# Kernel tuning notes

Measured on AMD Instinct MI355X. Metric: run time of the kernel, lower is better.

## Reference

```python
import jax, jax.numpy as jnp
import numpy as np

N = 50000       # nodes
E = 800000      # edges (before self-loops)
IN_DIM = 256
HID = 64
HEADS = 3
N_CLASSES = 40
NEG_SLOPE = 0.2  # PyG GATConv default negative_slope


def setup_inputs() -> dict:
    key = jax.random.key(0)
    ks = jax.random.split(key, 12)
    x = jax.random.normal(ks[0], (N, IN_DIM), jnp.float32)
    src = jax.random.randint(ks[1], (E,), 0, N, dtype=jnp.int32)
    off = jax.random.randint(ks[2], (E,), 1, N, dtype=jnp.int32)
    dst = (src + off) % N  # guarantees no self-loops
    edge_index = jnp.stack([src, dst], axis=0)
    g = 0.1
    W1 = jax.random.normal(ks[3], (IN_DIM, HEADS * HID), jnp.float32) * g
    att_src1 = jax.random.normal(ks[4], (HEADS, HID), jnp.float32) * g
    att_dst1 = jax.random.normal(ks[5], (HEADS, HID), jnp.float32) * g
    b1 = jnp.zeros((HEADS * HID,), jnp.float32)
    W2 = jax.random.normal(ks[6], (HEADS * HID, HEADS * HID), jnp.float32) * g
    att_src2 = jax.random.normal(ks[7], (HEADS, HID), jnp.float32) * g
    att_dst2 = jax.random.normal(ks[8], (HEADS, HID), jnp.float32) * g
    b2 = jnp.zeros((HEADS * HID,), jnp.float32)
    Wout = jax.random.normal(ks[9], (HEADS * HID, N_CLASSES), jnp.float32) * g
    bout = jnp.zeros((N_CLASSES,), jnp.float32)
    return {"x": x, "edge_index": edge_index,
            "W1": W1, "att_src1": att_src1, "att_dst1": att_dst1, "b1": b1,
            "W2": W2, "att_src2": att_src2, "att_dst2": att_dst2, "b2": b2,
            "Wout": Wout, "bout": bout}


def _segment_softmax(logits, seg, num_segments):
    # logits: [E', H], seg: [E'] destination node ids
    m = jax.ops.segment_max(logits, seg, num_segments=num_segments)
    e = jnp.exp(logits - m[seg])
    s = jax.ops.segment_sum(e, seg, num_segments=num_segments)
    return e / s[seg]


def _gat_layer(x, src, dst, W, att_src, att_dst, bias):
    n = x.shape[0]
    h = (x @ W).reshape(n, HEADS, HID)               # lin_src == lin_dst (x is a Tensor)
    a_src = jnp.sum(h * att_src, axis=-1)            # [N, H]
    a_dst = jnp.sum(h * att_dst, axis=-1)            # [N, H]
    alpha = jax.nn.leaky_relu(a_src[src] + a_dst[dst], NEG_SLOPE)  # [E', H]
    alpha = _segment_softmax(alpha, dst, n)
    msg = h[src] * alpha[:, :, None]                 # [E', H, C]
    out = jax.ops.segment_sum(msg, dst, num_segments=n)  # scatter-add aggregate
    return out.reshape(n, HEADS * HID) + bias        # concat heads + bias


def reference(x, edge_index, W1, att_src1, att_dst1, b1,
              W2, att_src2, att_dst2, b2, Wout, bout):
    n = x.shape[0]
    loop = jnp.arange(n, dtype=edge_index.dtype)
    src = jnp.concatenate([edge_index[0], loop])     # add_self_loops=True
    dst = jnp.concatenate([edge_index[1], loop])
    h = _gat_layer(x, src, dst, W1, att_src1, att_dst1, b1)
    h = jax.nn.relu(h)                               # dropout p=0 -> identity
    h = _gat_layer(h, src, dst, W2, att_src2, att_dst2, b2)
    h = jax.nn.relu(h)
    return h @ Wout + bout                           # node-level readout + outlayer
```

## Files before the change

### kernel.cpp

```cpp
#include <hip/hip_runtime.h>
#include <math.h>

#define NN 50000
#define NE 800000
#define KIN 256
#define F 192
#define NH 3
#define NC 40
#define CNT_BLKS ((NE+255)/256)
#define CONV_N (F*KIN + F*F + 48*F)
#define CONV_BLKS ((CONV_N+255)/256)
#define GEMM_GRID_C ((NN+63)/64)
#define EMIT_BLKS 49

typedef unsigned short u16;
typedef unsigned int   u32;
typedef __attribute__((ext_vector_type(8))) short bf16x8;
typedef __attribute__((ext_vector_type(4))) float f32x4;

static __device__ __forceinline__ u16 f2bf(float f){
  u32 u = __float_as_uint(f);
  u32 r = (u + 0x7fffu + ((u >> 16) & 1u)) >> 16;
  return (u16)r;
}

__global__ void count_conv_kernel(const int* __restrict__ dst, int* __restrict__ cnt,
                                  const float* __restrict__ W1, const float* __restrict__ W2,
                                  const float* __restrict__ Wout,
                                  u16* __restrict__ w1t, u16* __restrict__ w2t, u16* __restrict__ wot){
  int b = blockIdx.x;
  if (b < CNT_BLKS){
    int e = b*256 + threadIdx.x;
    if (e < NE) atomicAdd(&cnt[dst[e]], 1);
    return;
  }
  int e = (b - CNT_BLKS)*256 + threadIdx.x;
  if (e < F*KIN){
    int c = e / KIN, r = e % KIN;
    w1t[e] = f2bf(W1[(size_t)r*F + c]);
    return;
  }
  int e2 = e - F*KIN;
  if (e2 < F*F){
    int c = e2 / F, r = e2 % F;
    w2t[e2] = f2bf(W2[(size_t)r*F + c]);
    return;
  }
  int e3 = e2 - F*F;
  if (e3 < 48*F){
    int n = e3 / F, k = e3 % F;
    wot[e3] = (n < NC)? f2bf(Wout[(size_t)k*NC + n]) : (u16)0;
  }
}

__global__ __launch_bounds__(256) void emit_all(int* __restrict__ cnt, int* __restrict__ row_ptr){
  __shared__ int ts[256];
  __shared__ int s_pred;
  const int b = blockIdx.x, t = threadIdx.x;
  const int lim = b*1024;
  int pred = 0;
  for (int i = t*4; i < lim; i += 1024){
    int4 v = *(const int4*)&cnt[i];
    pred += v.x + v.y + v.z + v.w;
  }
  ts[t] = pred;
  __syncthreads();
  for (int off=128; off; off>>=1){
    if (t < off) ts[t] += ts[t+off];
    __syncthreads();
  }
  if (t == 0) s_pred = ts[0];
  __syncthreads();
  const int base = lim + t*4;
  int4 v = make_int4(0,0,0,0);
  if (base + 3 < NN) v = *(const int4*)&cnt[base];
  else if (base < NN){
    v.x = cnt[base];
    if (base+1 < NN) v.y = cnt[base+1];
    if (base+2 < NN) v.z = cnt[base+2];
  }
  int tot = v.x + v.y + v.z + v.w;
  ts[t] = tot;
  __syncthreads();
  #pragma unroll
  for (int off=1; off<256; off<<=1){
    int val = (t >= off)? ts[t-off] : 0;
    __syncthreads();
    ts[t] += val;
    __syncthreads();
  }
  int off0 = s_pred + ts[t] - tot;
  if (base + 3 < NN){
    row_ptr[base]   = off0;
    row_ptr[base+1] = off0 + v.x;
    row_ptr[base+2] = off0 + v.x + v.y;
    row_ptr[base+3] = off0 + v.x + v.y + v.z;
    *(int4*)&cnt[base] = make_int4(0,0,0,0);
  } else if (base < NN){
    row_ptr[base] = off0; cnt[base] = 0;
    if (base+1 < NN){ row_ptr[base+1] = off0 + v.x; cnt[base+1] = 0; }
    if (base+2 < NN){ row_ptr[base+2] = off0 + v.x + v.y; cnt[base+2] = 0; }
  }
  if (b == 0 && t == 0) row_ptr[NN] = NE;
}

#define SAK 72
#define SC  196
template<int K, bool CONVA, bool FILL>
__global__ __launch_bounds__(256) void gemm_mfma(const void* __restrict__ Araw, const u16* __restrict__ Bt,
                                                 u16* __restrict__ C,
                                                 const float* __restrict__ att_src, const float* __restrict__ att_dst,
                                                 float* __restrict__ a_src4, float* __restrict__ a_dst4,
                                                 const int* __restrict__ fsrc, const int* __restrict__ fdst,
                                                 const int* __restrict__ row_ptr, int* __restrict__ cur,
                                                 int* __restrict__ col){
  if (FILL && blockIdx.x >= GEMM_GRID_C){
    int e = (blockIdx.x - GEMM_GRID_C)*256 + threadIdx.x;
    if (e < NE){
      int d = fdst[e];
      int p = row_ptr[d] + atomicAdd(&cur[d], 1);
      col[p] = fsrc[e];
    }
    return;
  }
  __shared__ __align__(16) union {
    struct { u16 As[64*SAK]; u16 Bs[192*SAK]; } st;
    u16 Cs[64*SC];
  } sh;
  const int t = threadIdx.x;
  const int wave = t >> 6, lane = t & 63;
  const int quad = lane >> 4, l16 = lane & 15;
  const int r0 = blockIdx.x*64;

  f32x4 acc[4][3];
  #pragma unroll
  for (int rt=0;rt<4;rt++)
    #pragma unroll
    for (int ct=0;ct<3;ct++) acc[rt][ct] = (f32x4){0.f,0.f,0.f,0.f};

  for (int k0=0; k0<K; k0+=64){
    __syncthreads();
    {
      int row = t >> 2, kq = (t & 3)*16;
      bool ok = (r0+row) < NN;
      if (CONVA){
        const float* Af = (const float*)Araw;
        float4 v0 = make_float4(0,0,0,0), v1 = v0, v2 = v0, v3 = v0;
        if (ok){
          const float* p = &Af[(size_t)(r0+row)*K + k0 + kq];
          v0 = *(const float4*)(p+0);
          v1 = *(const float4*)(p+4);
          v2 = *(const float4*)(p+8);
          v3 = *(const float4*)(p+12);
        }
        uint4 pa, pb;
        pa.x = (u32)f2bf(v0.x) | ((u32)f2bf(v0.y) << 16);
        pa.y = (u32)f2bf(v0.z) | ((u32)f2bf(v0.w) << 16);
        pa.z = (u32)f2bf(v1.x) | ((u32)f2bf(v1.y) << 16);
        pa.w = (u32)f2bf(v1.z) | ((u32)f2bf(v1.w) << 16);
        pb.x = (u32)f2bf(v2.x) | ((u32)f2bf(v2.y) << 16);
        pb.y = (u32)f2bf(v2.z) | ((u32)f2bf(v2.w) << 16);
        pb.z = (u32)f2bf(v3.x) | ((u32)f2bf(v3.y) << 16);
        pb.w = (u32)f2bf(v3.z) | ((u32)f2bf(v3.w) << 16);
        *(uint4*)&sh.st.As[row*SAK + kq]     = pa;
        *(uint4*)&sh.st.As[row*SAK + kq + 8] = pb;
      } else {
        const u16* Ab = (const u16*)Araw;
        uint4 va = make_uint4(0,0,0,0), vb = va;
        if (ok){
          va = *(const uint4*)&Ab[(size_t)(r0+row)*K + k0 + kq];
          vb = *(const uint4*)&Ab[(size_t)(r0+row)*K + k0 + kq + 8];
        }
        *(uint4*)&sh.st.As[row*SAK + kq]     = va;
        *(uint4*)&sh.st.As[row*SAK + kq + 8] = vb;
      }
    }
    #pragma unroll
    for (int i=0;i<6;i++){
      int idx = t + i*256;
      int n = idx >> 3, kc = idx & 7;
      *(uint4*)&sh.st.Bs[n*SAK + kc*8] = *(const uint4*)&Bt[(size_t)n*K + k0 + kc*8];
    }
    __syncthreads();
    bf16x8 af[4][2], bf[3][2];
    #pragma unroll
    for (int kf=0;kf<2;kf++){
      #pragma unroll
      for (int rt=0;rt<4;rt++) af[rt][kf] = *(const bf16x8*)&sh.st.As[(rt*16 + l16)*SAK + kf*32 + quad*8];
      #pragma unroll
      for (int ct=0;ct<3;ct++) bf[ct][kf] = *(const bf16x8*)&sh.st.Bs[(wave*48 + ct*16 + l16)*SAK + kf*32 + quad*8];
    }
    #pragma unroll
    for (int kf=0;kf<2;kf++)
      #pragma unroll
      for (int rt=0;rt<4;rt++)
        #pragma unroll
        for (int ct=0;ct<3;ct++)
          acc[rt][ct] = __builtin_amdgcn_mfma_f32_16x16x32_bf16(af[rt][kf], bf[ct][kf], acc[rt][ct], 0, 0, 0);
  }

  __syncthreads();
  #pragma unroll
  for (int ct=0;ct<3;ct++){
    const int n = wave*48 + ct*16 + l16;
    #pragma unroll
    for (int rt=0;rt<4;rt++){
      #pragma unroll
      for (int reg=0;reg<4;reg++){
        const int m = rt*16 + quad*4 + reg;
        sh.Cs[m*SC + n] = f2bf(acc[rt][ct][reg]);
      }
    }
  }
  __syncthreads();
  {
    int row = t >> 2, c0 = (t & 3)*6;
    int grow = r0 + row;
    if (grow < NN){
      #pragma unroll
      for (int j=0;j<6;j++){
        int ch = c0 + j;
        uint4 v = *(const uint4*)&sh.Cs[row*SC + ch*8];
        *(uint4*)&C[(size_t)grow*F + ch*8] = v;
      }
    }
  }
  if (t < 192){
    int row = t & 63, head = t >> 6;
    int grow = r0 + row;
    if (grow < NN){
      float ps = 0.f, pd = 0.f;
      #pragma unroll
      for (int j=0;j<8;j++){
        uint4 v = *(const uint4*)&sh.Cs[row*SC + head*64 + j*8];
        float4 w0 = *(const float4*)&att_src[head*64 + j*8];
        float4 w1 = *(const float4*)&att_src[head*64 + j*8 + 4];
        float4 d0 = *(const float4*)&att_dst[head*64 + j*8];
        float4 d1 = *(const float4*)&att_dst[head*64 + j*8 + 4];
        float c0f = __uint_as_float(v.x << 16), c1f = __uint_as_float(v.x & 0xffff0000u);
        float c2f = __uint_as_float(v.y << 16), c3f = __uint_as_float(v.y & 0xffff0000u);
        float c4f = __uint_as_float(v.z << 16), c5f = __uint_as_float(v.z & 0xffff0000u);
        float c6f = __uint_as_float(v.w << 16), c7f = __uint_as_float(v.w & 0xffff0000u);
        ps = fmaf(c0f,w0.x,fmaf(c1f,w0.y,fmaf(c2f,w0.z,fmaf(c3f,w0.w,ps))));
        ps = fmaf(c4f,w1.x,fmaf(c5f,w1.y,fmaf(c6f,w1.z,fmaf(c7f,w1.w,ps))));
        pd = fmaf(c0f,d0.x,fmaf(c1f,d0.y,fmaf(c2f,d0.z,fmaf(c3f,d0.w,pd))));
        pd = fmaf(c4f,d1.x,fmaf(c5f,d1.y,fmaf(c6f,d1.z,fmaf(c7f,d1.w,pd))));
      }
      a_src4[(size_t)grow*4 + head] = ps;
      a_dst4[(size_t)grow*4 + head] = pd;
    }
  }
}

__global__ __launch_bounds__(256) void gat_agg_wave(const u16* __restrict__ hb,
    const float* __restrict__ a_src4, const float* __restrict__ a_dst4,
    const int* __restrict__ row_ptr, const int* __restrict__ col,
    const float* __restrict__ bias, u16* __restrict__ out){
  __shared__ float s_al[4][64][4];
  const int t = threadIdx.x;
  const int lane = t & 63;
  const int w = t >> 6;
  const int d = blockIdx.x*4 + w;
  if (d >= NN) return;
  const int e0  = row_ptr[d];
  const int deg = row_ptr[d+1] - e0;
  const int ecount = deg + 1;
  const float4 ad = *(const float4*)&a_dst4[(size_t)d*4];

  const int cg = (lane < 48)? lane : lane - 48;
  const int hg = (lane < 48)? (lane >> 4) : 0;
  const int cgo = cg*4;
  float4 acc = make_float4(0.f,0.f,0.f,0.f);
  float sl0=0.f, sl1=0.f, sl2=0.f;

  for (int base=0; base<ecount; base+=64){
    int j = base + lane;
    bool valid = j < ecount;
    int sn = d;
    if (j < deg) sn = col[e0+j];
    float4 as = *(const float4*)&a_src4[(size_t)sn*4];
    float l0 = as.x + ad.x; l0 = (l0>0.f)? l0 : 0.2f*l0;
    float l1 = as.y + ad.y; l1 = (l1>0.f)? l1 : 0.2f*l1;
    float l2 = as.z + ad.z; l2 = (l2>0.f)? l2 : 0.2f*l2;
    float E0 = valid? __expf(l0) : 0.f;
    float E1 = valid? __expf(l1) : 0.f;
    float E2 = valid? __expf(l2) : 0.f;
    sl0 += E0; sl1 += E1; sl2 += E2;
    float4 st; st.x = E0; st.y = E1; st.z = E2; st.w = 0.f;
    *(float4*)&s_al[w][lane][0] = st;
    __builtin_amdgcn_wave_barrier();
    int cnt = ecount - base; if (cnt > 64) cnt = 64;
    int jj = 0;
    for (; jj+4 <= cnt; jj += 4){
      int sA = __builtin_amdgcn_readlane(sn, jj);
      int sB = __builtin_amdgcn_readlane(sn, jj+1);
      int sC = __builtin_amdgcn_readlane(sn, jj+2);
      int sD = __builtin_amdgcn_readlane(sn, jj+3);
      uint2 pA = *(const uint2*)(hb + sA*F + cgo);
      uint2 pB = *(const uint2*)(hb + sB*F + cgo);
      uint2 pC = *(const uint2*)(hb + sC*F + cgo);
      uint2 pD = *(const uint2*)(hb + sD*F + cgo);
      float aA = s_al[w][jj  ][hg];
      float aB = s_al[w][jj+1][hg];
      float aC = s_al[w][jj+2][hg];
      float aD = s_al[w][jj+3][hg];
      acc.x = fmaf(aA, __uint_as_float(pA.x << 16),         acc.x);
      acc.y = fmaf(aA, __uint_as_float(pA.x & 0xffff0000u), acc.y);
      acc.z = fmaf(aA, __uint_as_float(pA.y << 16),         acc.z);
      acc.w = fmaf(aA, __uint_as_float(pA.y & 0xffff0000u), acc.w);
      acc.x = fmaf(aB, __uint_as_float(pB.x << 16),         acc.x);
      acc.y = fmaf(aB, __uint_as_float(pB.x & 0xffff0000u), acc.y);
      acc.z = fmaf(aB, __uint_as_float(pB.y << 16),         acc.z);
      acc.w = fmaf(aB, __uint_as_float(pB.y & 0xffff0000u), acc.w);
      acc.x = fmaf(aC, __uint_as_float(pC.x << 16),         acc.x);
      acc.y = fmaf(aC, __uint_as_float(pC.x & 0xffff0000u), acc.y);
      acc.z = fmaf(aC, __uint_as_float(pC.y << 16),         acc.z);
      acc.w = fmaf(aC, __uint_as_float(pC.y & 0xffff0000u), acc.w);
      acc.x = fmaf(aD, __uint_as_float(pD.x << 16),         acc.x);
      acc.y = fmaf(aD, __uint_as_float(pD.x & 0xffff0000u), acc.y);
      acc.z = fmaf(aD, __uint_as_float(pD.y << 16),         acc.z);
      acc.w = fmaf(aD, __uint_as_float(pD.y & 0xffff0000u), acc.w);
    }
    for (; jj < cnt; jj++){
      int sA = __builtin_amdgcn_readlane(sn, jj);
      uint2 pA = *(const uint2*)(hb + sA*F + cgo);
      float aA = s_al[w][jj][hg];
      acc.x = fmaf(aA, __uint_as_float(pA.x << 16),         acc.x);
      acc.y = fmaf(aA, __uint_as_float(pA.x & 0xffff0000u), acc.y);
      acc.z = fmaf(aA, __uint_as_float(pA.y << 16),         acc.z);
      acc.w = fmaf(aA, __uint_as_float(pA.y & 0xffff0000u), acc.w);
    }
    __builtin_amdgcn_wave_barrier();
  }
  #pragma unroll
  for (int off=32; off; off>>=1){
    sl0 += __shfl_xor(sl0, off);
    sl1 += __shfl_xor(sl1, off);
    sl2 += __shfl_xor(sl2, off);
  }
  if (lane < 48){
    float inv = 1.f / ((hg==0)? sl0 : ((hg==1)? sl1 : sl2));
    float4 b4 = *(const float4*)&bias[cg*4];
    uint2 o;
    o.x = (u32)f2bf(fmaxf(fmaf(acc.x, inv, b4.x), 0.f))
        | ((u32)f2bf(fmaxf(fmaf(acc.y, inv, b4.y), 0.f)) << 16);
    o.y = (u32)f2bf(fmaxf(fmaf(acc.z, inv, b4.z), 0.f))
        | ((u32)f2bf(fmaxf(fmaf(acc.w, inv, b4.w), 0.f)) << 16);
    *(uint2*)&out[(size_t)d*F + cg*4] = o;
  }
}

__global__ __launch_bounds__(256) void gemm_out_mfma(const u16* __restrict__ A,
    const u16* __restrict__ Wt, const float* __restrict__ bias, float* __restrict__ out){
  const int t = threadIdx.x;
  const int wave = t >> 6, lane = t & 63;
  const int quad = lane >> 4, l16 = lane & 15;
  const int rbase = blockIdx.x*64 + wave*16;
  const int arow = rbase + l16;
  f32x4 acc[3];
  #pragma unroll
  for (int ct=0;ct<3;ct++) acc[ct] = (f32x4){0.f,0.f,0.f,0.f};
  #pragma unroll
  for (int ks=0; ks<6; ks++){
    const int k0 = ks*32;
    union { uint4 u; bf16x8 h; } cva;
    cva.u = make_uint4(0,0,0,0);
    if (arow < NN) cva.u = *(const uint4*)&A[(size_t)arow*F + k0 + quad*8];
    #pragma unroll
    for (int ct=0;ct<3;ct++){
      bf16x8 bfr = *(const bf16x8*)&Wt[(size_t)(ct*16 + l16)*F + k0 + quad*8];
      acc[ct] = __builtin_amdgcn_mfma_f32_16x16x32_bf16(cva.h, bfr, acc[ct], 0, 0, 0);
    }
  }
  #pragma unroll
  for (int ct=0;ct<3;ct++){
    const int n = ct*16 + l16;
    #pragma unroll
    for (int reg=0;reg<4;reg++){
      const int m = quad*4 + reg;
      const int grow = rbase + m;
      if (grow < NN && n < NC) out[(size_t)grow*NC + n] = acc[ct][reg] + bias[n];
    }
  }
}

extern "C" void kernel_launch(void* const* d_in, const int* in_sizes, int n_in,
                              void* d_out, int out_size, void* d_ws, size_t ws_size,
                              hipStream_t stream){
  const float* x    = (const float*)d_in[0];
  const int*   ei   = (const int*)  d_in[1];
  const float* W1   = (const float*)d_in[2];
  const float* as1  = (const float*)d_in[3];
  const float* ad1  = (const float*)d_in[4];
  const float* b1   = (const float*)d_in[5];
  const float* W2   = (const float*)d_in[6];
  const float* as2  = (const float*)d_in[7];
  const float* ad2  = (const float*)d_in[8];
  const float* b2   = (const float*)d_in[9];
  const float* Wout = (const float*)d_in[10];
  const float* bout = (const float*)d_in[11];
  float* out = (float*)d_out;

  u16* w1t = (u16*)d_ws;
  u16* w2t = w1t + (size_t)F*KIN;
  u16* wot = w2t + (size_t)F*F;
  u16* hb1 = wot + (size_t)48*F;
  u16* hb2 = hb1 + (size_t)NN*F;
  u16* gb1 = hb2 + (size_t)NN*F;
  u16* gb2 = gb1 + (size_t)NN*F;
  float* a_src4 = (float*)(gb2 + (size_t)NN*F);
  float* a_dst4 = a_src4 + (size_t)NN*4;
  int* row_ptr  = (int*)(a_dst4 + (size_t)NN*4);
  int* col      = row_ptr + (NN+1);
  int* cnt      = col + NE;

  const int* srcv = ei;
  const int* dstv = ei + NE;

  hipMemsetAsync(cnt, 0, NN*sizeof(int), stream);
  count_conv_kernel<<<CNT_BLKS + CONV_BLKS, 256, 0, stream>>>(dstv, cnt, W1, W2, Wout, w1t, w2t, wot);
  emit_all<<<EMIT_BLKS, 256, 0, stream>>>(cnt, row_ptr);

  const int AGG_GRID = (NN + 3)/4;
  gemm_mfma<KIN,true,true><<<GEMM_GRID_C + CNT_BLKS, 256, 0, stream>>>(
      x, w1t, hb1, as1, ad1, a_src4, a_dst4, srcv, dstv, row_ptr, cnt, col);
  gat_agg_wave<<<AGG_GRID, 256, 0, stream>>>(hb1, a_src4, a_dst4, row_ptr, col, b1, gb1);
  gemm_mfma<F,false,false><<<GEMM_GRID_C, 256, 0, stream>>>(
      gb1, w2t, hb2, as2, ad2, a_src4, a_dst4, nullptr, nullptr, nullptr, nullptr, nullptr);
  gat_agg_wave<<<AGG_GRID, 256, 0, stream>>>(hb2, a_src4, a_dst4, row_ptr, col, b2, gb2);
  gemm_out_mfma<<<GEMM_GRID_C, 256, 0, stream>>>(gb2, wot, bout, out);
}
```

Measured before the change: 338.5 us.

## Pre-pack weights into MFMA fragment layout and load B directly from global

The weight conversion kernel now writes W1 and W2 in a k-blocked packed layout (groups of 8 k values per output column), so each lane can fetch its bf16x8 B fragment with one global load. The GEMM kernel stops staging B tiles in shared memory, which shrinks LDS use and removes the B store/load traffic. B fragments are issued before the A staging so their latency can overlap it. The cost is that each wave reads B from global/L2 independently instead of sharing it through LDS.

```diff
diff --git a/kernel.cpp b/kernel.cpp
--- a/kernel.cpp
+++ b/kernel.cpp
@@ -8,7 +8,7 @@
 #define NH 3
 #define NC 40
 #define CNT_BLKS ((NE+255)/256)
-#define CONV_N (F*KIN + F*F + 48*F)
+#define CONV_N (KIN*F + F*F + 48*F)
 #define CONV_BLKS ((CONV_N+255)/256)
 #define GEMM_GRID_C ((NN+63)/64)
 #define EMIT_BLKS 49
@@ -27,7 +27,7 @@
 __global__ void count_conv_kernel(const int* __restrict__ dst, int* __restrict__ cnt,
                                   const float* __restrict__ W1, const float* __restrict__ W2,
                                   const float* __restrict__ Wout,
-                                  u16* __restrict__ w1t, u16* __restrict__ w2t, u16* __restrict__ wot){
+                                  u16* __restrict__ w1p, u16* __restrict__ w2p, u16* __restrict__ wot){
   int b = blockIdx.x;
   if (b < CNT_BLKS){
     int e = b*256 + threadIdx.x;
@@ -35,15 +35,15 @@
     return;
   }
   int e = (b - CNT_BLKS)*256 + threadIdx.x;
-  if (e < F*KIN){
-    int c = e / KIN, r = e % KIN;
-    w1t[e] = f2bf(W1[(size_t)r*F + c]);
+  if (e < KIN*F){
+    int k = e / F, n = e % F;
+    w1p[((size_t)(k>>3)*F + n)*8 + (k&7)] = f2bf(W1[e]);
     return;
   }
-  int e2 = e - F*KIN;
+  int e2 = e - KIN*F;
   if (e2 < F*F){
-    int c = e2 / F, r = e2 % F;
-    w2t[e2] = f2bf(W2[(size_t)r*F + c]);
+    int k = e2 / F, n = e2 % F;
+    w2p[((size_t)(k>>3)*F + n)*8 + (k&7)] = f2bf(W2[e2]);
     return;
   }
   int e3 = e2 - F*F;
@@ -107,7 +107,7 @@
 #define SAK 72
 #define SC  196
 template<int K, bool CONVA, bool FILL>
-__global__ __launch_bounds__(256) void gemm_mfma(const void* __restrict__ Araw, const u16* __restrict__ Bt,
+__global__ __launch_bounds__(256) void gemm_mfma(const void* __restrict__ Araw, const u16* __restrict__ Bp,
                                                  u16* __restrict__ C,
                                                  const float* __restrict__ att_src, const float* __restrict__ att_dst,
                                                  float* __restrict__ a_src4, float* __restrict__ a_dst4,
@@ -124,7 +124,7 @@
     return;
   }
   __shared__ __align__(16) union {
-    struct { u16 As[64*SAK]; u16 Bs[192*SAK]; } st;
+    u16 As[64*SAK];
     u16 Cs[64*SC];
   } sh;
   const int t = threadIdx.x;
@@ -138,8 +138,18 @@
     #pragma unroll
     for (int ct=0;ct<3;ct++) acc[rt][ct] = (f32x4){0.f,0.f,0.f,0.f};
 
+  const u16* Bl = Bp + (size_t)(wave*48 + l16)*8;
+
   for (int k0=0; k0<K; k0+=64){
     __syncthreads();
+    bf16x8 bf[3][2];
+    #pragma unroll
+    for (int kf=0;kf<2;kf++){
+      const size_t kb = (size_t)((k0>>3) + kf*4 + quad)*F*8;
+      #pragma unroll
+      for (int ct=0;ct<3;ct++)
+        bf[ct][kf] = *(const bf16x8*)&Bl[kb + ct*16*8];
+    }
     {
       int row = t >> 2, kq = (t & 3)*16;
       bool ok = (r0+row) < NN;
@@ -162,8 +172,8 @@
         pb.y = (u32)f2bf(v2.z) | ((u32)f2bf(v2.w) << 16);
         pb.z = (u32)f2bf(v3.x) | ((u32)f2bf(v3.y) << 16);
         pb.w = (u32)f2bf(v3.z) | ((u32)f2bf(v3.w) << 16);
-        *(uint4*)&sh.st.As[row*SAK + kq]     = pa;
-        *(uint4*)&sh.st.As[row*SAK + kq + 8] = pb;
+        *(uint4*)&sh.As[row*SAK + kq]     = pa;
+        *(uint4*)&sh.As[row*SAK + kq + 8] = pb;
       } else {
         const u16* Ab = (const u16*)Araw;
         uint4 va = make_uint4(0,0,0,0), vb = va;
@@ -171,25 +181,16 @@
           va = *(const uint4*)&Ab[(size_t)(r0+row)*K + k0 + kq];
           vb = *(const uint4*)&Ab[(size_t)(r0+row)*K + k0 + kq + 8];
         }
-        *(uint4*)&sh.st.As[row*SAK + kq]     = va;
-        *(uint4*)&sh.st.As[row*SAK + kq + 8] = vb;
+        *(uint4*)&sh.As[row*SAK + kq]     = va;
+        *(uint4*)&sh.As[row*SAK + kq + 8] = vb;
       }
     }
-    #pragma unroll
-    for (int i=0;i<6;i++){
-      int idx = t + i*256;
-      int n = idx >> 3, kc = idx & 7;
-      *(uint4*)&sh.st.Bs[n*SAK + kc*8] = *(const uint4*)&Bt[(size_t)n*K + k0 + kc*8];
-    }
     __syncthreads();
-    bf16x8 af[4][2], bf[3][2];
-    #pragma unroll
-    for (int kf=0;kf<2;kf++){
-      #pragma unroll
-      for (int rt=0;rt<4;rt++) af[rt][kf] = *(const bf16x8*)&sh.st.As[(rt*16 + l16)*SAK + kf*32 + quad*8];
-      #pragma unroll
-      for (int ct=0;ct<3;ct++) bf[ct][kf] = *(const bf16x8*)&sh.st.Bs[(wave*48 + ct*16 + l16)*SAK + kf*32 + quad*8];
-    }
+    bf16x8 af[4][2];
+    #pragma unroll
+    for (int kf=0;kf<2;kf++)
+      #pragma unroll
+      for (int rt=0;rt<4;rt++) af[rt][kf] = *(const bf16x8*)&sh.As[(rt*16 + l16)*SAK + kf*32 + quad*8];
     #pragma unroll
     for (int kf=0;kf<2;kf++)
       #pragma unroll
@@ -401,9 +402,9 @@
   const float* bout = (const float*)d_in[11];
   float* out = (float*)d_out;
 
-  u16* w1t = (u16*)d_ws;
-  u16* w2t = w1t + (size_t)F*KIN;
-  u16* wot = w2t + (size_t)F*F;
+  u16* w1p = (u16*)d_ws;
+  u16* w2p = w1p + (size_t)KIN*F;
+  u16* wot = w2p + (size_t)F*F;
   u16* hb1 = wot + (size_t)48*F;
   u16* hb2 = hb1 + (size_t)NN*F;
   u16* gb1 = hb2 + (size_t)NN*F;
@@ -418,15 +419,15 @@
   const int* dstv = ei + NE;
 
   hipMemsetAsync(cnt, 0, NN*sizeof(int), stream);
-  count_conv_kernel<<<CNT_BLKS + CONV_BLKS, 256, 0, stream>>>(dstv, cnt, W1, W2, Wout, w1t, w2t, wot);
+  count_conv_kernel<<<CNT_BLKS + CONV_BLKS, 256, 0, stream>>>(dstv, cnt, W1, W2, Wout, w1p, w2p, wot);
   emit_all<<<EMIT_BLKS, 256, 0, stream>>>(cnt, row_ptr);
 
   const int AGG_GRID = (NN + 3)/4;
   gemm_mfma<KIN,true,true><<<GEMM_GRID_C + CNT_BLKS, 256, 0, stream>>>(
-      x, w1t, hb1, as1, ad1, a_src4, a_dst4, srcv, dstv, row_ptr, cnt, col);
+      x, w1p, hb1, as1, ad1, a_src4, a_dst4, srcv, dstv, row_ptr, cnt, col);
   gat_agg_wave<<<AGG_GRID, 256, 0, stream>>>(hb1, a_src4, a_dst4, row_ptr, col, b1, gb1);
   gemm_mfma<F,false,false><<<GEMM_GRID_C, 256, 0, stream>>>(
-      gb1, w2t, hb2, as2, ad2, a_src4, a_dst4, nullptr, nullptr, nullptr, nullptr, nullptr);
+      gb1, w2p, hb2, as2, ad2, a_src4, a_dst4, nullptr, nullptr, nullptr, nullptr, nullptr);
   gat_agg_wave<<<AGG_GRID, 256, 0, stream>>>(hb2, a_src4, a_dst4, row_ptr, col, b2, gb2);
   gemm_out_mfma<<<GEMM_GRID_C, 256, 0, stream>>>(gb2, wot, bout, out);
 }
```

Measured after the change: 338.8 us. Within noise of the previous version (+0.1%).
